# Performance work log

Measured on AMD Instinct MI355X. Metric: run time of the kernel, lower is better.

Reference implementation:

```python
import jax, jax.numpy as jnp
import numpy as np

HIDDEN_DIM = 64
VOCAB_SIZE = 128
NUM_SLOTS = 64
B, L = 256, 4096


def layer_norm(x, gamma, beta, eps=1e-5):
    mu = jnp.mean(x, axis=-1, keepdims=True)
    var = jnp.mean(jnp.square(x - mu), axis=-1, keepdims=True)
    return (x - mu) * jax.lax.rsqrt(var + eps) * gamma + beta


def _l2norm(x, axis=-1, eps=1e-12):
    # matches torch F.normalize: x / max(||x||, eps)
    n = jnp.sqrt(jnp.sum(jnp.square(x), axis=axis, keepdims=True))
    return x / jnp.maximum(n, eps)


def setup_inputs() -> dict:
    key = jax.random.key(0)
    ks = jax.random.split(key, 13)
    H, V, S = HIDDEN_DIM, VOCAB_SIZE, NUM_SLOTS
    return {
        "seq": jax.random.randint(ks[0], (B, L), 0, V),
        "embed_w": jax.random.normal(ks[1], (V, H), dtype=jnp.float32),
        # linear weights stored [in, out] (transposed vs torch)
        "w1": jax.random.normal(ks[2], (H, 2 * H), dtype=jnp.float32) * 0.05,
        "b1": jnp.zeros((2 * H,), dtype=jnp.float32),
        "w2": jax.random.normal(ks[3], (2 * H, H), dtype=jnp.float32) * 0.05,
        "b2": jnp.zeros((H,), dtype=jnp.float32),
        "ln_g": jnp.ones((H,), dtype=jnp.float32),
        "ln_b": jnp.zeros((H,), dtype=jnp.float32),
        "slot_keys": jax.random.normal(ks[4], (S, H), dtype=jnp.float32) * 0.1,
        "slot_vals": jax.random.normal(ks[5], (S, H), dtype=jnp.float32) * 0.1,
        "gate_w": jax.random.normal(ks[6], (H, S), dtype=jnp.float32) * 0.05,
        "gate_b": jnp.zeros((S,), dtype=jnp.float32),
        "out_w": jax.random.normal(ks[7], (H, V), dtype=jnp.float32) * 0.05,
        "out_b": jnp.zeros((V,), dtype=jnp.float32),
    }


def reference(seq, embed_w, w1, b1, w2, b2, ln_g, ln_b,
              slot_keys, slot_vals, gate_w, gate_b, out_w, out_b):
    h = embed_w[seq]                                   # [B, L, H]
    ff = jnp.maximum(h @ w1 + b1, 0.0) @ w2 + b2       # [B, L, H]
    h = layer_norm(h + ff, ln_g, ln_b)

    hw = h[:, :-1, :]                                  # written tokens [B, L-1, H]
    w = jax.nn.softmax(hw @ gate_w + gate_b, axis=-1)  # [B, L-1, S]
    # the per-step increment w_t (outer) h_t is independent of prior keys,
    # so the sequential loop collapses exactly to one contraction:
    keys = slot_keys[None, :, :] + jnp.einsum('btn,bth->bnh', w, hw)  # [B, S, H]
    vals = keys  # loop sets vals = keys every step; L > 1 here

    q = h[:, -1, :]                                    # [B, H]
    sim = jnp.einsum('bnh,bh->bn', _l2norm(keys), _l2norm(q))
    attn = jax.nn.softmax(sim, axis=-1)                # [B, S]
    ctx = jnp.einsum('bn,bnh->bh', attn, vals)         # [B, H]
    return ctx @ out_w + out_b                         # [B, V]
```

## Files before the change

kernel.cpp:

```cpp
#include <hip/hip_runtime.h>

#define HD 64
#define VC 128
#define NS 64
#define NB 256
#define SL 4096

__device__ __forceinline__ float wsum(float x) {
#pragma unroll
  for (int o = 32; o > 0; o >>= 1) x += __shfl_xor(x, o, 64);
  return x;
}
__device__ __forceinline__ float wmax(float x) {
#pragma unroll
  for (int o = 32; o > 0; o >>= 1) x = fmaxf(x, __shfl_xor(x, o, 64));
  return x;
}

__global__ __launch_bounds__(128) void build_tables(
    const float* __restrict__ embed, const float* __restrict__ w1, const float* __restrict__ b1,
    const float* __restrict__ w2, const float* __restrict__ b2,
    const float* __restrict__ ln_g, const float* __restrict__ ln_b,
    const float* __restrict__ gate_w, const float* __restrict__ gate_b,
    float* __restrict__ HN, float* __restrict__ WSM)
{
  const int v = blockIdx.x, t = threadIdx.x;
  __shared__ float s_e[HD], s_f1[2 * HD], s_hn[HD], s_red[128];

  if (t < HD) s_e[t] = embed[v * HD + t];
  __syncthreads();

  {
    float a0 = 0.f, a1 = 0.f, a2 = 0.f, a3 = 0.f;
#pragma unroll
    for (int h = 0; h < HD; h += 4) {
      a0 = fmaf(s_e[h + 0], w1[(h + 0) * 2 * HD + t], a0);
      a1 = fmaf(s_e[h + 1], w1[(h + 1) * 2 * HD + t], a1);
      a2 = fmaf(s_e[h + 2], w1[(h + 2) * 2 * HD + t], a2);
      a3 = fmaf(s_e[h + 3], w1[(h + 3) * 2 * HD + t], a3);
    }
    s_f1[t] = fmaxf(b1[t] + ((a0 + a1) + (a2 + a3)), 0.f);
  }
  __syncthreads();

  {
    const int col = t & 63;
    const int j0 = (t >> 6) << 6;
    float a0 = 0.f, a1 = 0.f, a2 = 0.f, a3 = 0.f;
#pragma unroll
    for (int j = 0; j < 64; j += 4) {
      a0 = fmaf(s_f1[j0 + j + 0], w2[(j0 + j + 0) * HD + col], a0);
      a1 = fmaf(s_f1[j0 + j + 1], w2[(j0 + j + 1) * HD + col], a1);
      a2 = fmaf(s_f1[j0 + j + 2], w2[(j0 + j + 2) * HD + col], a2);
      a3 = fmaf(s_f1[j0 + j + 3], w2[(j0 + j + 3) * HD + col], a3);
    }
    s_red[t] = (a0 + a1) + (a2 + a3);
  }
  __syncthreads();

  if (t < HD) {
    float x = s_e[t] + b2[t] + s_red[t] + s_red[t + 64];
    float mu = wsum(x) * (1.f / 64.f);
    float d = x - mu;
    float var = wsum(d * d) * (1.f / 64.f);
    float hn = d * rsqrtf(var + 1e-5f) * ln_g[t] + ln_b[t];
    s_hn[t] = hn;
    HN[v * HD + t] = hn;
  }
  __syncthreads();

  {
    const int col = t & 63;
    const int hh0 = (t >> 6) << 5;
    float a0 = 0.f, a1 = 0.f, a2 = 0.f, a3 = 0.f;
#pragma unroll
    for (int h = 0; h < 32; h += 4) {
      a0 = fmaf(s_hn[hh0 + h + 0], gate_w[(hh0 + h + 0) * NS + col], a0);
      a1 = fmaf(s_hn[hh0 + h + 1], gate_w[(hh0 + h + 1) * NS + col], a1);
      a2 = fmaf(s_hn[hh0 + h + 2], gate_w[(hh0 + h + 2) * NS + col], a2);
      a3 = fmaf(s_hn[hh0 + h + 3], gate_w[(hh0 + h + 3) * NS + col], a3);
    }
    s_red[t] = (a0 + a1) + (a2 + a3);
  }
  __syncthreads();

  if (t < NS) {
    float g = gate_b[t] + s_red[t] + s_red[t + 64];
    float m = wmax(g);
    float e = expf(g - m);
    float s = wsum(e);
    WSM[v * NS + t] = e / s;
  }
}

__global__ __launch_bounds__(1024) void batch_kernel(
    const int* __restrict__ seq, const float* __restrict__ HN, const float* __restrict__ WSM,
    const float* __restrict__ slot_keys, const float* __restrict__ out_w,
    const float* __restrict__ out_b, float* __restrict__ out)
{
  const int b = blockIdx.x, t = threadIdx.x;
  const int lane = t & 63, wave = t >> 6;

  __shared__ int s_cnt[VC];
  __shared__ int s_qtok;
  __align__(16) __shared__ float s_hn[VC * HD];
  __align__(16) __shared__ float s_wsm[VC * NS];
  __align__(16) __shared__ float s_keys[NS * HD];
  __align__(16) __shared__ float s_part[16 * HD];
  __shared__ float s_q[HD], s_sim[NS], s_ctx[HD];

  const int qt = t >> 8;
  const int tid = t & 255;
  const int n0 = (tid >> 4) << 2;
  const int h0 = (tid & 15) << 2;

  float4 sk0, sk1, sk2, sk3;
  if (qt == 0) {
    sk0 = *(const float4*)&slot_keys[(n0 + 0) * HD + h0];
    sk1 = *(const float4*)&slot_keys[(n0 + 1) * HD + h0];
    sk2 = *(const float4*)&slot_keys[(n0 + 2) * HD + h0];
    sk3 = *(const float4*)&slot_keys[(n0 + 3) * HD + h0];
  }

  if (t < VC) s_cnt[t] = 0;
  __syncthreads();

  const int* sb = seq + b * SL;
  const int4 sv = ((const int4*)sb)[t];
  const float4 h0v = ((const float4*)HN)[t];
  const float4 h1v = ((const float4*)HN)[t + 1024];
  const float4 g0v = ((const float4*)WSM)[t];
  const float4 g1v = ((const float4*)WSM)[t + 1024];
  atomicAdd(&s_cnt[sv.x], 1);
  atomicAdd(&s_cnt[sv.y], 1);
  atomicAdd(&s_cnt[sv.z], 1);
  if (t != 1023) atomicAdd(&s_cnt[sv.w], 1);
  else s_qtok = sv.w;
  ((float4*)s_hn)[t] = h0v;
  ((float4*)s_hn)[t + 1024] = h1v;
  __syncthreads();

  {
    const float c0 = (float)s_cnt[t >> 4];
    const float c1 = (float)s_cnt[(t + 1024) >> 4];
    float4 a = g0v, c = g1v;
    a.x *= c0; a.y *= c0; a.z *= c0; a.w *= c0;
    c.x *= c1; c.y *= c1; c.z *= c1; c.w *= c1;
    ((float4*)s_wsm)[t] = a;
    ((float4*)s_wsm)[t + 1024] = c;
  }
  if (t < HD) s_q[t] = s_hn[s_qtok * HD + t];
  __syncthreads();

  const float* hb = s_hn + qt * 32 * HD;
  const float* wb = s_wsm + qt * 32 * NS;

  float accv[4][4];
  if (qt == 0) {
    accv[0][0] = sk0.x; accv[0][1] = sk0.y; accv[0][2] = sk0.z; accv[0][3] = sk0.w;
    accv[1][0] = sk1.x; accv[1][1] = sk1.y; accv[1][2] = sk1.z; accv[1][3] = sk1.w;
    accv[2][0] = sk2.x; accv[2][1] = sk2.y; accv[2][2] = sk2.z; accv[2][3] = sk2.w;
    accv[3][0] = sk3.x; accv[3][1] = sk3.y; accv[3][2] = sk3.z; accv[3][3] = sk3.w;
  } else {
#pragma unroll
    for (int r = 0; r < 4; ++r)
#pragma unroll
      for (int c = 0; c < 4; ++c) accv[r][c] = 0.f;
  }

#pragma unroll 4
  for (int v = 0; v < 32; ++v) {
    const float4 hv = *(const float4*)&hb[v * HD + h0];
    const float4 wv = *(const float4*)&wb[v * NS + n0];
    accv[0][0] = fmaf(wv.x, hv.x, accv[0][0]);
    accv[0][1] = fmaf(wv.x, hv.y, accv[0][1]);
    accv[0][2] = fmaf(wv.x, hv.z, accv[0][2]);
    accv[0][3] = fmaf(wv.x, hv.w, accv[0][3]);
    accv[1][0] = fmaf(wv.y, hv.x, accv[1][0]);
    accv[1][1] = fmaf(wv.y, hv.y, accv[1][1]);
    accv[1][2] = fmaf(wv.y, hv.z, accv[1][2]);
    accv[1][3] = fmaf(wv.y, hv.w, accv[1][3]);
    accv[2][0] = fmaf(wv.z, hv.x, accv[2][0]);
    accv[2][1] = fmaf(wv.z, hv.y, accv[2][1]);
    accv[2][2] = fmaf(wv.z, hv.z, accv[2][2]);
    accv[2][3] = fmaf(wv.z, hv.w, accv[2][3]);
    accv[3][0] = fmaf(wv.w, hv.x, accv[3][0]);
    accv[3][1] = fmaf(wv.w, hv.y, accv[3][1]);
    accv[3][2] = fmaf(wv.w, hv.z, accv[3][2]);
    accv[3][3] = fmaf(wv.w, hv.w, accv[3][3]);
  }
  __syncthreads();

  float* kA = s_hn;
  float* kB = s_hn + NS * HD;
  if (qt == 1) {
#pragma unroll
    for (int r = 0; r < 4; ++r) {
      float4 st; st.x = accv[r][0]; st.y = accv[r][1]; st.z = accv[r][2]; st.w = accv[r][3];
      *(float4*)&kA[(n0 + r) * HD + h0] = st;
    }
  } else if (qt == 3) {
#pragma unroll
    for (int r = 0; r < 4; ++r) {
      float4 st; st.x = accv[r][0]; st.y = accv[r][1]; st.z = accv[r][2]; st.w = accv[r][3];
      *(float4*)&kB[(n0 + r) * HD + h0] = st;
    }
  }
  __syncthreads();
  if (qt == 0) {
#pragma unroll
    for (int r = 0; r < 4; ++r) {
      float4 p = *(const float4*)&kA[(n0 + r) * HD + h0];
      p.x += accv[r][0]; p.y += accv[r][1]; p.z += accv[r][2]; p.w += accv[r][3];
      *(float4*)&kA[(n0 + r) * HD + h0] = p;
    }
  } else if (qt == 2) {
#pragma unroll
    for (int r = 0; r < 4; ++r) {
      float4 p = *(const float4*)&kB[(n0 + r) * HD + h0];
      p.x += accv[r][0]; p.y += accv[r][1]; p.z += accv[r][2]; p.w += accv[r][3];
      *(float4*)&kB[(n0 + r) * HD + h0] = p;
    }
  }
  __syncthreads();
  {
    float4 a = ((const float4*)kA)[t];
    const float4 c = ((const float4*)kB)[t];
    a.x += c.x; a.y += c.y; a.z += c.z; a.w += c.w;
    ((float4*)s_keys)[t] = a;
  }
  __syncthreads();

  const float qv = s_q[lane];
  const float qn = fmaxf(sqrtf(wsum(qv * qv)), 1e-12f);
#pragma unroll
  for (int r = 0; r < 4; ++r) {
    const int n = (wave << 2) + r;
    const float kv = s_keys[n * HD + lane];
    const float kk = wsum(kv * kv);
    const float kq = wsum(kv * qv);
    if (lane == 0) s_sim[n] = kq / (fmaxf(sqrtf(kk), 1e-12f) * qn);
  }
  __syncthreads();

  {
    const float svv = s_sim[lane];
    const float m = wmax(svv);
    const float e = expf(svv - m);
    const float ssum = wsum(e);
    const float attn_l = e / ssum;
    float c = 0.f;
#pragma unroll
    for (int r = 0; r < 4; ++r) {
      const int n = (wave << 2) + r;
      const float an = __shfl(attn_l, n, 64);
      c = fmaf(an, s_keys[n * HD + lane], c);
    }
    s_part[wave * HD + lane] = c;
  }
  __syncthreads();
  if (wave == 0) {
    float c0 = 0.f, c1 = 0.f, c2 = 0.f, c3 = 0.f;
#pragma unroll
    for (int w = 0; w < 16; w += 4) {
      c0 += s_part[(w + 0) * HD + lane];
      c1 += s_part[(w + 1) * HD + lane];
      c2 += s_part[(w + 2) * HD + lane];
      c3 += s_part[(w + 3) * HD + lane];
    }
    s_ctx[lane] = (c0 + c1) + (c2 + c3);
  }
  __syncthreads();

  if (t < VC) {
    float o0 = 0.f, o1 = 0.f, o2 = 0.f, o3 = 0.f;
#pragma unroll
    for (int h = 0; h < HD; h += 4) {
      o0 = fmaf(s_ctx[h + 0], out_w[(h + 0) * VC + t], o0);
      o1 = fmaf(s_ctx[h + 1], out_w[(h + 1) * VC + t], o1);
      o2 = fmaf(s_ctx[h + 2], out_w[(h + 2) * VC + t], o2);
      o3 = fmaf(s_ctx[h + 3], out_w[(h + 3) * VC + t], o3);
    }
    out[b * VC + t] = out_b[t] + ((o0 + o1) + (o2 + o3));
  }
}

extern "C" void kernel_launch(void* const* d_in, const int* in_sizes, int n_in,
                              void* d_out, int out_size, void* d_ws, size_t ws_size,
                              hipStream_t stream) {
  const int* seq         = (const int*)d_in[0];
  const float* embed_w   = (const float*)d_in[1];
  const float* w1        = (const float*)d_in[2];
  const float* b1        = (const float*)d_in[3];
  const float* w2        = (const float*)d_in[4];
  const float* b2        = (const float*)d_in[5];
  const float* ln_g      = (const float*)d_in[6];
  const float* ln_b      = (const float*)d_in[7];
  const float* slot_keys = (const float*)d_in[8];
  const float* gate_w    = (const float*)d_in[10];
  const float* gate_b    = (const float*)d_in[11];
  const float* out_w     = (const float*)d_in[12];
  const float* out_b     = (const float*)d_in[13];
  float* out = (float*)d_out;

  float* HN  = (float*)d_ws;
  float* WSM = HN + VC * HD;

  build_tables<<<VC, 128, 0, stream>>>(embed_w, w1, b1, w2, b2, ln_g, ln_b,
                                       gate_w, gate_b, HN, WSM);
  batch_kernel<<<NB, 1024, 0, stream>>>(seq, HN, WSM, slot_keys, out_w, out_b, out);
}
```

Before: 93.64 us.

## Compute slot-key contraction with split-bf16 MFMA on transposed swizzled LDS tiles

Replaces the scalar-FMA count-weighted contraction (64x64 output over 128 vocab entries, split four ways with a multi-stage shared-memory reduction) with MFMA 16x16x32 bf16 instructions. Each fp32 operand is split into hi/lo bf16 parts and three-plus cross products are accumulated to keep near-fp32 accuracy. Operands are stored transposed in XOR-swizzled LDS to avoid bank conflicts, and the partial-sum reduction barriers disappear. Risks are the accuracy of the bf16 split and the cost of the extra conversion work relative to a very small matmul.

```diff
diff --git a/kernel.cpp b/kernel.cpp
--- a/kernel.cpp
+++ b/kernel.cpp
@@ -5,6 +5,11 @@
 #define NS 64
 #define NB 256
 #define SL 4096
+
+typedef __attribute__((ext_vector_type(8))) short short8;
+typedef __attribute__((ext_vector_type(4))) float f32x4;
+
+#define SWZ(row, col_u) ((((row) * VC) + (col_u)) ^ (((row) & 7) << 3))
 
 __device__ __forceinline__ float wsum(float x) {
 #pragma unroll
@@ -103,131 +108,99 @@
 
   __shared__ int s_cnt[VC];
   __shared__ int s_qtok;
-  __align__(16) __shared__ float s_hn[VC * HD];
-  __align__(16) __shared__ float s_wsm[VC * NS];
+  __align__(16) __shared__ unsigned short s_wt_hi[NS * VC];
+  __align__(16) __shared__ unsigned short s_wt_lo[NS * VC];
+  __align__(16) __shared__ unsigned short s_ht_hi[HD * VC];
+  __align__(16) __shared__ unsigned short s_ht_lo[HD * VC];
   __align__(16) __shared__ float s_keys[NS * HD];
   __align__(16) __shared__ float s_part[16 * HD];
   __shared__ float s_q[HD], s_sim[NS], s_ctx[HD];
 
-  const int qt = t >> 8;
-  const int tid = t & 255;
-  const int n0 = (tid >> 4) << 2;
-  const int h0 = (tid & 15) << 2;
-
-  float4 sk0, sk1, sk2, sk3;
-  if (qt == 0) {
-    sk0 = *(const float4*)&slot_keys[(n0 + 0) * HD + h0];
-    sk1 = *(const float4*)&slot_keys[(n0 + 1) * HD + h0];
-    sk2 = *(const float4*)&slot_keys[(n0 + 2) * HD + h0];
-    sk3 = *(const float4*)&slot_keys[(n0 + 3) * HD + h0];
-  }
-
-  if (t < VC) s_cnt[t] = 0;
-  __syncthreads();
+  const int col64 = t & 63;
+  const int vb = t >> 6;
+
+  const int n0 = (wave & 3) << 4;
+  const int h0 = (wave >> 2) << 4;
+  const int fr = lane & 15;
+  const int fg = lane >> 4;
 
   const int* sb = seq + b * SL;
   const int4 sv = ((const int4*)sb)[t];
-  const float4 h0v = ((const float4*)HN)[t];
-  const float4 h1v = ((const float4*)HN)[t + 1024];
-  const float4 g0v = ((const float4*)WSM)[t];
-  const float4 g1v = ((const float4*)WSM)[t + 1024];
+
+  float wreg[8], hreg[8];
+#pragma unroll
+  for (int j = 0; j < 8; ++j) {
+    wreg[j] = WSM[(vb * 8 + j) * NS + col64];
+    hreg[j] = HN[(vb * 8 + j) * HD + col64];
+  }
+  float skv[4];
+#pragma unroll
+  for (int r = 0; r < 4; ++r)
+    skv[r] = slot_keys[(n0 + fg * 4 + r) * HD + h0 + fr];
+
+  if (t < VC) s_cnt[t] = 0;
+  __syncthreads();
+
   atomicAdd(&s_cnt[sv.x], 1);
   atomicAdd(&s_cnt[sv.y], 1);
   atomicAdd(&s_cnt[sv.z], 1);
   if (t != 1023) atomicAdd(&s_cnt[sv.w], 1);
   else s_qtok = sv.w;
-  ((float4*)s_hn)[t] = h0v;
-  ((float4*)s_hn)[t + 1024] = h1v;
-  __syncthreads();
-
-  {
-    const float c0 = (float)s_cnt[t >> 4];
-    const float c1 = (float)s_cnt[(t + 1024) >> 4];
-    float4 a = g0v, c = g1v;
-    a.x *= c0; a.y *= c0; a.z *= c0; a.w *= c0;
-    c.x *= c1; c.y *= c1; c.z *= c1; c.w *= c1;
-    ((float4*)s_wsm)[t] = a;
-    ((float4*)s_wsm)[t + 1024] = c;
-  }
-  if (t < HD) s_q[t] = s_hn[s_qtok * HD + t];
-  __syncthreads();
-
-  const float* hb = s_hn + qt * 32 * HD;
-  const float* wb = s_wsm + qt * 32 * NS;
-
-  float accv[4][4];
-  if (qt == 0) {
-    accv[0][0] = sk0.x; accv[0][1] = sk0.y; accv[0][2] = sk0.z; accv[0][3] = sk0.w;
-    accv[1][0] = sk1.x; accv[1][1] = sk1.y; accv[1][2] = sk1.z; accv[1][3] = sk1.w;
-    accv[2][0] = sk2.x; accv[2][1] = sk2.y; accv[2][2] = sk2.z; accv[2][3] = sk2.w;
-    accv[3][0] = sk3.x; accv[3][1] = sk3.y; accv[3][2] = sk3.z; accv[3][3] = sk3.w;
-  } else {
+  __syncthreads();
+
+  {
+    short8 vwhi, vwlo, vhhi, vhlo;
+#pragma unroll
+    for (int j = 0; j < 8; ++j) {
+      const float c = (float)s_cnt[vb * 8 + j];
+      const float w = wreg[j] * c;
+      const unsigned int wb_ = __float_as_uint(w);
+      vwhi[j] = (short)(wb_ >> 16);
+      const float wr = w - __uint_as_float(wb_ & 0xffff0000u);
+      vwlo[j] = (short)(__float_as_uint(wr) >> 16);
+
+      const float h = hreg[j];
+      const unsigned int hb_ = __float_as_uint(h);
+      vhhi[j] = (short)(hb_ >> 16);
+      const float hr = h - __uint_as_float(hb_ & 0xffff0000u);
+      vhlo[j] = (short)(__float_as_uint(hr) >> 16);
+    }
+    const int idx = SWZ(col64, vb * 8);
+    *(short8*)&s_wt_hi[idx] = vwhi;
+    *(short8*)&s_wt_lo[idx] = vwlo;
+    *(short8*)&s_ht_hi[idx] = vhhi;
+    *(short8*)&s_ht_lo[idx] = vhlo;
+  }
+  {
+    const int qtok = s_qtok;
+    if (vb == (qtok >> 3)) {
+      const int qj = qtok & 7;
+      float qv = hreg[0];
+#pragma unroll
+      for (int j = 1; j < 8; ++j) if (qj == j) qv = hreg[j];
+      s_q[col64] = qv;
+    }
+  }
+  __syncthreads();
+
+  {
+    f32x4 acc = {skv[0], skv[1], skv[2], skv[3]};
+#pragma unroll
+    for (int kc = 0; kc < 4; ++kc) {
+      const int au = SWZ(n0 + fr, fg * 8 + kc * 32);
+      const int bu = SWZ(h0 + fr, fg * 8 + kc * 32);
+      const short8 ahi = *(const short8*)&s_wt_hi[au];
+      const short8 alo = *(const short8*)&s_wt_lo[au];
+      const short8 bhi = *(const short8*)&s_ht_hi[bu];
+      const short8 blo = *(const short8*)&s_ht_lo[bu];
+      acc = __builtin_amdgcn_mfma_f32_16x16x32_bf16(ahi, bhi, acc, 0, 0, 0);
+      acc = __builtin_amdgcn_mfma_f32_16x16x32_bf16(ahi, blo, acc, 0, 0, 0);
+      acc = __builtin_amdgcn_mfma_f32_16x16x32_bf16(alo, bhi, acc, 0, 0, 0);
+      acc = __builtin_amdgcn_mfma_f32_16x16x32_bf16(alo, blo, acc, 0, 0, 0);
+    }
 #pragma unroll
     for (int r = 0; r < 4; ++r)
-#pragma unroll
-      for (int c = 0; c < 4; ++c) accv[r][c] = 0.f;
-  }
-
-#pragma unroll 4
-  for (int v = 0; v < 32; ++v) {
-    const float4 hv = *(const float4*)&hb[v * HD + h0];
-    const float4 wv = *(const float4*)&wb[v * NS + n0];
-    accv[0][0] = fmaf(wv.x, hv.x, accv[0][0]);
-    accv[0][1] = fmaf(wv.x, hv.y, accv[0][1]);
-    accv[0][2] = fmaf(wv.x, hv.z, accv[0][2]);
-    accv[0][3] = fmaf(wv.x, hv.w, accv[0][3]);
-    accv[1][0] = fmaf(wv.y, hv.x, accv[1][0]);
-    accv[1][1] = fmaf(wv.y, hv.y, accv[1][1]);
-    accv[1][2] = fmaf(wv.y, hv.z, accv[1][2]);
-    accv[1][3] = fmaf(wv.y, hv.w, accv[1][3]);
-    accv[2][0] = fmaf(wv.z, hv.x, accv[2][0]);
-    accv[2][1] = fmaf(wv.z, hv.y, accv[2][1]);
-    accv[2][2] = fmaf(wv.z, hv.z, accv[2][2]);
-    accv[2][3] = fmaf(wv.z, hv.w, accv[2][3]);
-    accv[3][0] = fmaf(wv.w, hv.x, accv[3][0]);
-    accv[3][1] = fmaf(wv.w, hv.y, accv[3][1]);
-    accv[3][2] = fmaf(wv.w, hv.z, accv[3][2]);
-    accv[3][3] = fmaf(wv.w, hv.w, accv[3][3]);
-  }
-  __syncthreads();
-
-  float* kA = s_hn;
-  float* kB = s_hn + NS * HD;
-  if (qt == 1) {
-#pragma unroll
-    for (int r = 0; r < 4; ++r) {
-      float4 st; st.x = accv[r][0]; st.y = accv[r][1]; st.z = accv[r][2]; st.w = accv[r][3];
-      *(float4*)&kA[(n0 + r) * HD + h0] = st;
-    }
-  } else if (qt == 3) {
-#pragma unroll
-    for (int r = 0; r < 4; ++r) {
-      float4 st; st.x = accv[r][0]; st.y = accv[r][1]; st.z = accv[r][2]; st.w = accv[r][3];
-      *(float4*)&kB[(n0 + r) * HD + h0] = st;
-    }
-  }
-  __syncthreads();
-  if (qt == 0) {
-#pragma unroll
-    for (int r = 0; r < 4; ++r) {
-      float4 p = *(const float4*)&kA[(n0 + r) * HD + h0];
-      p.x += accv[r][0]; p.y += accv[r][1]; p.z += accv[r][2]; p.w += accv[r][3];
-      *(float4*)&kA[(n0 + r) * HD + h0] = p;
-    }
-  } else if (qt == 2) {
-#pragma unroll
-    for (int r = 0; r < 4; ++r) {
-      float4 p = *(const float4*)&kB[(n0 + r) * HD + h0];
-      p.x += accv[r][0]; p.y += accv[r][1]; p.z += accv[r][2]; p.w += accv[r][3];
-      *(float4*)&kB[(n0 + r) * HD + h0] = p;
-    }
-  }
-  __syncthreads();
-  {
-    float4 a = ((const float4*)kA)[t];
-    const float4 c = ((const float4*)kB)[t];
-    a.x += c.x; a.y += c.y; a.z += c.z; a.w += c.w;
-    ((float4*)s_keys)[t] = a;
+      s_keys[(n0 + fg * 4 + r) * HD + h0 + fr] = acc[r];
   }
   __syncthreads();
 
```

Result: no change. 92.05 us (-1.7%).
